# Performance work log

Hardware: AMD Instinct MI355X
Metric: run time of the kernel (lower is better)

Reference implementation:

```python
import jax, jax.numpy as jnp
import numpy as np

NUM_NODES = 100000
HIDDEN = 128
HEADS = 4
NUM_EDGES = 1600000
NUM_PAIRS = 100000


def _leaky_relu(x, slope=0.2):
    return jnp.where(x >= 0, x, slope * x)


def _gat_layer(x, W, a_src, a_dst, src, dst):
    # x: [N, D]; W: [D, H*Dh]; a_src/a_dst: [H, Dh]
    N = x.shape[0]
    H, Dh = a_src.shape
    h = (x @ W).reshape(N, H, Dh)
    hs = h[src]                                   # [E, H, Dh] gather
    e = _leaky_relu((hs * a_src).sum(-1) + (h[dst] * a_dst).sum(-1))  # [E, H]
    # torch scatter_reduce amax over a zeros buffer => max clamped at 0
    m = jnp.maximum(jax.ops.segment_max(e, dst, num_segments=N), 0.0)  # [N, H]
    a = jnp.exp(e - m[dst])
    s = jax.ops.segment_sum(a, dst, num_segments=N)
    a = a / (s[dst] + 1e-10)
    out = jax.ops.segment_sum(hs * a[..., None], dst, num_segments=N)  # [N, H, Dh]
    return out.reshape(N, H * Dh)


def setup_inputs() -> dict:
    key = jax.random.key(0)
    ks = jax.random.split(key, 16)
    N, D, H = NUM_NODES, HIDDEN, HEADS
    Dh = D // H
    sW = float(np.sqrt(6.0 / (D + D)))
    sa = float(np.sqrt(6.0 / (H + Dh)))
    inp = {
        'embed': jax.random.uniform(ks[0], (N, D), jnp.float32, -sW, sW),
        'W1': jax.random.uniform(ks[1], (D, D), jnp.float32, -sW, sW),
        'a_src1': jax.random.uniform(ks[2], (H, Dh), jnp.float32, -sa, sa),
        'a_dst1': jax.random.uniform(ks[3], (H, Dh), jnp.float32, -sa, sa),
        'W2': jax.random.uniform(ks[4], (D, D), jnp.float32, -sW, sW),
        'a_src2': jax.random.uniform(ks[5], (H, Dh), jnp.float32, -sa, sa),
        'a_dst2': jax.random.uniform(ks[6], (H, Dh), jnp.float32, -sa, sa),
        'lp_w1': jax.random.uniform(ks[7], (2 * D, D), jnp.float32, -sW, sW),
        'lp_b1': jnp.zeros((D,), jnp.float32),
        'lp_w2': jax.random.uniform(ks[8], (D, 1), jnp.float32, -sW, sW),
        'lp_b2': jnp.zeros((1,), jnp.float32),
        'edge_index': jax.random.randint(ks[9], (2, NUM_EDGES), 0, N, jnp.int64 if jax.config.jax_enable_x64 else jnp.int32),
        'link_src': jax.random.randint(ks[10], (NUM_PAIRS,), 0, N),
        'link_dst': jax.random.randint(ks[11], (NUM_PAIRS,), 0, N),
    }
    return inp


def reference(embed, W1, a_src1, a_dst1, W2, a_src2, a_dst2,
              lp_w1, lp_b1, lp_w2, lp_b2, edge_index, link_src, link_dst):
    src, dst = edge_index[0], edge_index[1]
    x = embed
    x = jax.nn.elu(_gat_layer(x, W1, a_src1, a_dst1, src, dst)) + x
    x = jax.nn.elu(_gat_layer(x, W2, a_src2, a_dst2, src, dst)) + x
    z = x
    hcat = jnp.concatenate([z[link_src], z[link_dst]], axis=-1)  # [P, 2D]
    hid = jax.nn.relu(hcat @ lp_w1 + lp_b1)
    logits = (hid @ lp_w2 + lp_b2).squeeze(-1)  # [P]
    return logits
```

## Files before the change

kernel.cpp:

```cpp
#include <hip/hip_runtime.h>

typedef unsigned short u16;
typedef unsigned int u32;
typedef __attribute__((ext_vector_type(8))) short short8;
typedef __attribute__((ext_vector_type(4))) float float4v;

#define N_NODES 100000
#define N_EDGES 1600000
#define N_PAIRS 100000
#define NBUCKP 256
#define NB_USED 196
#define BUCK_CAP 8704
#define BIN_GRID 391

__device__ __forceinline__ float bf2f(u32 lo16) {
    union { u32 u; float f; } v;
    v.u = lo16 << 16;
    return v.f;
}
__device__ __forceinline__ u16 f2bf(float f) {
    union { float f; u32 u; } v;
    v.f = f;
    u32 r = v.u + 0x7fffu + ((v.u >> 16) & 1u);
    return (u16)(r >> 16);
}

__global__ __launch_bounds__(256) void k_prepB4(const float* __restrict__ W1, const float* __restrict__ W2,
                                                const float* __restrict__ WA, const float* __restrict__ WB,
                                                u16* __restrict__ B1, u16* __restrict__ B2,
                                                u16* __restrict__ BA, u16* __restrict__ BB,
                                                int* __restrict__ bucket_cur) {
    if (blockIdx.x == 32) {
        bucket_cur[threadIdx.x] = threadIdx.x * BUCK_CAP;
        return;
    }
    int w = blockIdx.x >> 3;
    const float* W = (w == 0) ? W1 : (w == 1) ? W2 : (w == 2) ? WA : WB;
    u16* Bf = (w == 0) ? B1 : (w == 1) ? B2 : (w == 2) ? BA : BB;
    int t = (blockIdx.x & 7) * 256 + threadIdx.x;
    int kk = t >> 9, tn = (t >> 6) & 7, quad = (t >> 4) & 3, l15 = t & 15;
#pragma unroll
    for (int j = 0; j < 8; j++) {
        int k = kk * 32 + quad * 8 + j;
        int n = tn * 16 + l15;
        Bf[(size_t)t * 8 + j] = f2bf(W[k * 128 + n]);
    }
}

__global__ __launch_bounds__(256) void k_bin(const int* __restrict__ esrc, const int* __restrict__ edst,
                                             int* bucket_cur, int2* __restrict__ binned) {
    __shared__ int cnt[NBUCKP];
    __shared__ int base[NBUCKP];
    int t = threadIdx.x;
    cnt[t] = 0;
    __syncthreads();
    int s[16], d[16], r[16];
    int e0 = blockIdx.x * 4096;
#pragma unroll
    for (int k = 0; k < 16; k++) {
        int e = e0 + k * 256 + t;
        if (e < N_EDGES) {
            s[k] = esrc[e];
            d[k] = edst[e];
            r[k] = atomicAdd(&cnt[d[k] >> 9], 1);
        } else {
            d[k] = -1;
        }
    }
    __syncthreads();
    base[t] = cnt[t] ? atomicAdd(&bucket_cur[t], cnt[t]) : 0;
    __syncthreads();
#pragma unroll
    for (int k = 0; k < 16; k++) {
        if (d[k] >= 0) {
            int bk = d[k] >> 9;
            int pos = base[bk] + r[k];
            if (pos < (bk + 1) * BUCK_CAP)
                binned[pos] = make_int2(s[k], d[k]);
        }
    }
}

__global__ __launch_bounds__(512) void k_sort(const int2* __restrict__ binned,
                                              const int* __restrict__ bucket_cur,
                                              int* __restrict__ row_ptr,
                                              int* __restrict__ col_src) {
    __shared__ int cnt[512];
    __shared__ int sm[512];
    int b = blockIdx.x, t = threadIdx.x;

    int partial = 0;
    if (t < b) partial = bucket_cur[t] - t * BUCK_CAP;
    sm[t] = partial;
    __syncthreads();
    for (int o = 256; o >= 1; o >>= 1) {
        if (t < o) sm[t] += sm[t + o];
        __syncthreads();
    }
    int base = sm[0];
    int n_e = bucket_cur[b] - b * BUCK_CAP;
    if (n_e > BUCK_CAP) n_e = BUCK_CAP;
    __syncthreads();

    cnt[t] = 0;
    __syncthreads();
    const int2* ebase = binned + (size_t)b * BUCK_CAP;
    for (int i = t; i < n_e; i += 512)
        atomicAdd(&cnt[ebase[i].y & 511], 1);
    __syncthreads();
    int v = cnt[t];
    sm[t] = v;
    __syncthreads();
    for (int o = 1; o < 512; o <<= 1) {
        int x = (t >= o) ? sm[t - o] : 0;
        __syncthreads();
        sm[t] += x;
        __syncthreads();
    }
    int excl = base + sm[t] - v;
    int node = b * 512 + t;
    if (node <= N_NODES) row_ptr[node] = excl;
    cnt[t] = excl;
    __syncthreads();
    for (int i = t; i < n_e; i += 512) {
        int2 sd = ebase[i];
        int p = atomicAdd(&cnt[sd.y & 511], 1);
        col_src[p] = sd.x;
    }
}

template<bool AF32, bool DUAL, bool QUANT>
__global__ __launch_bounds__(256) void k_gemm(const void* __restrict__ Ap,
                                              const u16* __restrict__ Bf,
                                              const u16* __restrict__ Bf2,
                                              u16* __restrict__ C,
                                              u16* __restrict__ C2,
                                              char* __restrict__ hq,
                                              float* __restrict__ alsc,
                                              const float* __restrict__ a_src,
                                              const float* __restrict__ a_dst,
                                              float* __restrict__ al_d, int M) {
    int wave = threadIdx.x >> 6, lane = threadIdx.x & 63;
    int quad = lane >> 4, l15 = lane & 15;
    int row0 = blockIdx.x * 64 + wave * 16;
    int m = row0 + l15;
    int mload = (m < M) ? m : (M - 1);

    short8 a[4];
    if (AF32) {
        const float* A = (const float*)Ap;
#pragma unroll
        for (int kk = 0; kk < 4; kk++) {
            const float* p = A + (size_t)mload * 128 + kk * 32 + quad * 8;
            float4 f0 = *(const float4*)p;
            float4 f1 = *(const float4*)(p + 4);
            short8 av;
            av[0] = (short)f2bf(f0.x); av[1] = (short)f2bf(f0.y);
            av[2] = (short)f2bf(f0.z); av[3] = (short)f2bf(f0.w);
            av[4] = (short)f2bf(f1.x); av[5] = (short)f2bf(f1.y);
            av[6] = (short)f2bf(f1.z); av[7] = (short)f2bf(f1.w);
            a[kk] = av;
        }
    } else {
        const u16* A = (const u16*)Ap;
#pragma unroll
        for (int kk = 0; kk < 4; kk++)
            a[kk] = *(const short8*)(A + (size_t)mload * 128 + kk * 32 + quad * 8);
    }

    float4v acc[8], acc2[8];
#pragma unroll
    for (int tn = 0; tn < 8; tn++) {
        acc[tn] = (float4v){0.f, 0.f, 0.f, 0.f};
        if (DUAL) acc2[tn] = (float4v){0.f, 0.f, 0.f, 0.f};
    }

#pragma unroll
    for (int kk = 0; kk < 4; kk++) {
#pragma unroll
        for (int tn = 0; tn < 8; tn++) {
            short8 b = *(const short8*)(Bf + ((size_t)((kk * 8 + tn) * 64 + lane)) * 8);
            acc[tn] = __builtin_amdgcn_mfma_f32_16x16x32_bf16(a[kk], b, acc[tn], 0, 0, 0);
            if (DUAL) {
                short8 b2 = *(const short8*)(Bf2 + ((size_t)((kk * 8 + tn) * 64 + lane)) * 8);
                acc2[tn] = __builtin_amdgcn_mfma_f32_16x16x32_bf16(a[kk], b2, acc2[tn], 0, 0, 0);
            }
        }
    }

    float as0[4], as1[4], ad0[4], ad1[4];
    if (QUANT) {
#pragma unroll
        for (int hd = 0; hd < 4; hd++) {
            as0[hd] = a_src[hd * 32 + l15];
            as1[hd] = a_src[hd * 32 + 16 + l15];
            ad0[hd] = a_dst[hd * 32 + l15];
            ad1[hd] = a_dst[hd * 32 + 16 + l15];
        }
    }

#pragma unroll
    for (int rg = 0; rg < 4; rg++) {
        int gr = row0 + quad * 4 + rg;
        bool ok = (gr < M);
        if (!QUANT) {
            if (ok) {
#pragma unroll
                for (int tn = 0; tn < 8; tn++) {
                    C[(size_t)gr * 128 + tn * 16 + l15] = f2bf(acc[tn][rg]);
                    if (DUAL) C2[(size_t)gr * 128 + tn * 16 + l15] = f2bf(acc2[tn][rg]);
                }
            }
        } else {
            float amax = 0.f;
#pragma unroll
            for (int tn = 0; tn < 8; tn++) amax = fmaxf(amax, fabsf(acc[tn][rg]));
#pragma unroll
            for (int mm = 1; mm < 16; mm <<= 1) amax = fmaxf(amax, __shfl_xor(amax, mm, 64));
            float inv_s = (amax > 0.f) ? 127.f / amax : 0.f;
            if (ok) {
#pragma unroll
                for (int tn = 0; tn < 8; tn++) {
                    int q = (int)rintf(acc[tn][rg] * inv_s);
                    hq[(size_t)gr * 128 + tn * 16 + l15] = (char)q;
                }
                if (l15 == 0) alsc[(size_t)gr * 8 + 4] = amax * (1.f / 127.f);
            }
            float ps[4], pd[4];
#pragma unroll
            for (int hd = 0; hd < 4; hd++) {
                float c0 = acc[2 * hd][rg];
                float c1 = acc[2 * hd + 1][rg];
                ps[hd] = c0 * as0[hd] + c1 * as1[hd];
                pd[hd] = c0 * ad0[hd] + c1 * ad1[hd];
            }
#pragma unroll
            for (int mm = 1; mm < 16; mm <<= 1) {
#pragma unroll
                for (int hd = 0; hd < 4; hd++) {
                    ps[hd] += __shfl_xor(ps[hd], mm, 64);
                    pd[hd] += __shfl_xor(pd[hd], mm, 64);
                }
            }
            if (ok && l15 < 4) {
                float vs = (l15 == 0) ? ps[0] : (l15 == 1) ? ps[1] : (l15 == 2) ? ps[2] : ps[3];
                float vd = (l15 == 0) ? pd[0] : (l15 == 1) ? pd[1] : (l15 == 2) ? pd[2] : pd[3];
                alsc[(size_t)gr * 8 + l15] = vs;
                al_d[gr * 4 + l15] = vd;
            }
        }
    }
}

template<bool XF32>
__global__ __launch_bounds__(256) void k_agg(const int* __restrict__ row_ptr, const int* __restrict__ col_src,
                      const float* __restrict__ alsc, const float* __restrict__ al_d,
                      const char* __restrict__ hq,
                      const void* __restrict__ xin, u16* __restrict__ xout) {
    int node = blockIdx.x * 4 + (threadIdx.x >> 6);
    int lane = threadIdx.x & 63;
    int l15 = lane & 15;
    int grp = lane >> 4;
    int bh  = l15 >> 2;
    int ae  = lane >> 2;
    int ah  = lane & 3;
    int beg = row_ptr[node], end = row_ptr[node + 1];
    int deg = end - beg;
    int degm1 = (deg > 0) ? deg - 1 : 0;
    float adst = al_d[node * 4 + ah];
    const char* hrow = hq + l15 * 8;

    float sw = 0.f;
    float acc[8];
#pragma unroll
    for (int k = 0; k < 8; k++) acc[k] = 0.f;

    int nch = (deg + 15) >> 4;
    for (int cb = 0; cb < nch; cb++) {
        int c = cb * 16;
        int idx = c + l15;
        idx = (idx <= degm1) ? idx : degm1;
        int sv = col_src[beg + idx];

        int sA = __shfl(sv, ae, 64);
        const float* ap = alsc + (size_t)sA * 8;
        float ev = ap[ah] + adst;
        ev = fmaxf(ev, 0.2f * ev);
        float w = __expf(ev);
        w = ((c + ae) < deg) ? w : 0.f;
        sw += w;
        float wsc = w * ap[4];

#pragma unroll
        for (int i = 0; i < 4; i++) {
            int slot = 4 * i + grp;
            int s = __shfl(sv, slot, 64);
            float wl = __shfl(wsc, slot * 4 + bh, 64);
            uint2 hv = *(const uint2*)(hrow + (size_t)s * 128);
            acc[0] += wl * (float)(int)(signed char)(hv.x);
            acc[1] += wl * (float)(int)(signed char)(hv.x >> 8);
            acc[2] += wl * (float)(int)(signed char)(hv.x >> 16);
            acc[3] += wl * (float)(int)(signed char)(hv.x >> 24);
            acc[4] += wl * (float)(int)(signed char)(hv.y);
            acc[5] += wl * (float)(int)(signed char)(hv.y >> 8);
            acc[6] += wl * (float)(int)(signed char)(hv.y >> 16);
            acc[7] += wl * (float)(int)(signed char)(hv.y >> 24);
        }
    }

#pragma unroll
    for (int mm = 4; mm < 64; mm <<= 1) sw += __shfl_xor(sw, mm, 64);
    float inv = 1.f / (__shfl(sw, bh, 64) + 1e-10f);

#pragma unroll
    for (int k = 0; k < 8; k++) {
        acc[k] += __shfl_xor(acc[k], 16, 64);
        acc[k] += __shfl_xor(acc[k], 32, 64);
    }

    if (grp == 0) {
        float r[8];
        if (XF32) {
            const float* x = (const float*)xin;
            float4 x0 = *(const float4*)&x[(size_t)node * 128 + l15 * 8];
            float4 x1 = *(const float4*)&x[(size_t)node * 128 + l15 * 8 + 4];
            r[0] = x0.x; r[1] = x0.y; r[2] = x0.z; r[3] = x0.w;
            r[4] = x1.x; r[5] = x1.y; r[6] = x1.z; r[7] = x1.w;
        } else {
            const u16* x = (const u16*)xin;
            short8 xv = *(const short8*)&x[(size_t)node * 128 + l15 * 8];
#pragma unroll
            for (int k = 0; k < 8; k++) r[k] = bf2f((u16)xv[k]);
        }
        u32 ow[4];
#pragma unroll
        for (int k = 0; k < 4; k++) {
            float a0 = acc[2 * k] * inv;
            float a1 = acc[2 * k + 1] * inv;
            a0 = (a0 > 0.f) ? a0 : (__expf(a0) - 1.f);
            a1 = (a1 > 0.f) ? a1 : (__expf(a1) - 1.f);
            ow[k] = (u32)f2bf(a0 + r[2 * k]) | ((u32)f2bf(a1 + r[2 * k + 1]) << 16);
        }
        *(uint4*)&xout[(size_t)node * 128 + l15 * 8] = make_uint4(ow[0], ow[1], ow[2], ow[3]);
    }
}

__global__ void k_pair(const int* __restrict__ psrc, const int* __restrict__ pdst,
                       const u16* __restrict__ u, const u16* __restrict__ v,
                       const float* __restrict__ b1, const float* __restrict__ w2,
                       const float* __restrict__ b2, float* __restrict__ out) {
    int p = blockIdx.x * 4 + (threadIdx.x >> 6);
    int lane = threadIdx.x & 63;
    int s = psrc[p], d = pdst[p];
    float h0 = bf2f(u[(size_t)s * 128 + lane * 2])     + bf2f(v[(size_t)d * 128 + lane * 2])     + b1[lane * 2];
    float h1 = bf2f(u[(size_t)s * 128 + lane * 2 + 1]) + bf2f(v[(size_t)d * 128 + lane * 2 + 1]) + b1[lane * 2 + 1];
    h0 = (h0 > 0.f) ? h0 : 0.f;
    h1 = (h1 > 0.f) ? h1 : 0.f;
    float acc = h0 * w2[lane * 2] + h1 * w2[lane * 2 + 1];
#pragma unroll
    for (int m = 1; m < 64; m <<= 1) acc += __shfl_xor(acc, m, 64);
    if (lane == 0) out[p] = acc + b2[0];
}

extern "C" void kernel_launch(void* const* d_in, const int* in_sizes, int n_in,
                              void* d_out, int out_size, void* d_ws, size_t ws_size,
                              hipStream_t stream) {
    const float* embed  = (const float*)d_in[0];
    const float* W1     = (const float*)d_in[1];
    const float* a_src1 = (const float*)d_in[2];
    const float* a_dst1 = (const float*)d_in[3];
    const float* W2     = (const float*)d_in[4];
    const float* a_src2 = (const float*)d_in[5];
    const float* a_dst2 = (const float*)d_in[6];
    const float* lp_w1  = (const float*)d_in[7];
    const float* lp_b1  = (const float*)d_in[8];
    const float* lp_w2  = (const float*)d_in[9];
    const float* lp_b2  = (const float*)d_in[10];
    const int*   edge   = (const int*)d_in[11];
    const int*   lsrc   = (const int*)d_in[12];
    const int*   ldst   = (const int*)d_in[13];
    float* out = (float*)d_out;

    char* ws = (char*)d_ws;
    size_t off = 0;
    auto alloc = [&](size_t bytes) -> char* {
        char* p = ws + off;
        off += (bytes + 255) & ~(size_t)255;
        return p;
    };
    int*  row_ptr    = (int*)alloc((N_NODES + 1) * 4);
    int*  bucket_cur = (int*)alloc(NBUCKP * 4);
    int2* binned     = (int2*)alloc((size_t)NBUCKP * BUCK_CAP * 8);
    int*  col_src    = (int*)alloc((size_t)N_EDGES * 4);
    char* hq         = (char*)alloc((size_t)N_NODES * 128);
    float* alsc      = (float*)alloc((size_t)N_NODES * 8 * 4);
    float* al_d      = (float*)alloc((size_t)N_NODES * 4 * 4);
    u16*  x1         = (u16*)alloc((size_t)N_NODES * 128 * 2);
    u16*  z          = (u16*)alloc((size_t)N_NODES * 128 * 2);
    u16*  uu         = (u16*)alloc((size_t)N_NODES * 128 * 2);
    u16*  vv         = (u16*)alloc((size_t)N_NODES * 128 * 2);
    u16*  Bf1        = (u16*)alloc(128 * 128 * 2);
    u16*  Bf2        = (u16*)alloc(128 * 128 * 2);
    u16*  BfA        = (u16*)alloc(128 * 128 * 2);
    u16*  BfB        = (u16*)alloc(128 * 128 * 2);

    const int* esrc = edge;
    const int* edst = edge + N_EDGES;
    const int GB = (N_NODES + 63) / 64;

    k_prepB4<<<33, 256, 0, stream>>>(W1, W2, lp_w1, lp_w1 + 128 * 128, Bf1, Bf2, BfA, BfB, bucket_cur);

    k_bin <<<BIN_GRID, 256, 0, stream>>>(esrc, edst, bucket_cur, binned);
    k_sort<<<NB_USED, 512, 0, stream>>>(binned, bucket_cur, row_ptr, col_src);

    k_gemm<true, false, true><<<GB, 256, 0, stream>>>(embed, Bf1, nullptr, nullptr, nullptr,
                                                      hq, alsc, a_src1, a_dst1, al_d, N_NODES);
    k_agg<true><<<N_NODES / 4, 256, 0, stream>>>(row_ptr, col_src, alsc, al_d, hq, embed, x1);
    k_gemm<false, false, true><<<GB, 256, 0, stream>>>(x1, Bf2, nullptr, nullptr, nullptr,
                                                       hq, alsc, a_src2, a_dst2, al_d, N_NODES);
    k_agg<false><<<N_NODES / 4, 256, 0, stream>>>(row_ptr, col_src, alsc, al_d, hq, x1, z);
    k_gemm<false, true, false><<<GB, 256, 0, stream>>>(z, BfA, BfB, uu, vv,
                                                       nullptr, nullptr, nullptr, nullptr, nullptr, N_NODES);
    k_pair<<<N_PAIRS / 4, 256, 0, stream>>>(lsrc, ldst, uu, vv, lp_b1, lp_w2, lp_b2, out);
}
```

Before: 359.7 us.

## Use offset-int8 with fp16 magic-number unpack and v_fma_mix in aggregation

Stores quantized features with a +128 bias so that a byte permute with 0x64 produces fp16 values of 1024+128+q directly, avoiding per-byte sign-extension and int-to-float conversions. The weight is converted to fp16 once per load and accumulated with v_fma_mix_f32, and the constant offset (1152 times the weight sum) is subtracted at the end. The per-node scale is interleaved next to each head's attention logit so a single float2 load fetches both. Rounding the weight to fp16 and the large-offset cancellation reduce precision.

```diff
diff --git a/kernel.cpp b/kernel.cpp
--- a/kernel.cpp
+++ b/kernel.cpp
@@ -24,6 +24,9 @@
     u32 r = v.u + 0x7fffu + ((v.u >> 16) & 1u);
     return (u16)(r >> 16);
 }
+
+#define FMIX_LO(A, Q, W) asm("v_fma_mix_f32 %0, %1, %2, %0 op_sel:[0,0,0] op_sel_hi:[1,1,0]" : "+v"(A) : "v"(Q), "v"(W))
+#define FMIX_HI(A, Q, W) asm("v_fma_mix_f32 %0, %1, %2, %0 op_sel:[1,0,0] op_sel_hi:[1,1,0]" : "+v"(A) : "v"(Q), "v"(W))
 
 __global__ __launch_bounds__(256) void k_prepB4(const float* __restrict__ W1, const float* __restrict__ W2,
                                                 const float* __restrict__ WA, const float* __restrict__ WB,
@@ -222,9 +225,8 @@
 #pragma unroll
                 for (int tn = 0; tn < 8; tn++) {
                     int q = (int)rintf(acc[tn][rg] * inv_s);
-                    hq[(size_t)gr * 128 + tn * 16 + l15] = (char)q;
+                    hq[(size_t)gr * 128 + tn * 16 + l15] = (char)(q + 128);
                 }
-                if (l15 == 0) alsc[(size_t)gr * 8 + 4] = amax * (1.f / 127.f);
             }
             float ps[4], pd[4];
 #pragma unroll
@@ -245,7 +247,8 @@
             if (ok && l15 < 4) {
                 float vs = (l15 == 0) ? ps[0] : (l15 == 1) ? ps[1] : (l15 == 2) ? ps[2] : ps[3];
                 float vd = (l15 == 0) ? pd[0] : (l15 == 1) ? pd[1] : (l15 == 2) ? pd[2] : pd[3];
-                alsc[(size_t)gr * 8 + l15] = vs;
+                alsc[(size_t)gr * 8 + l15 * 2]     = vs;
+                alsc[(size_t)gr * 8 + l15 * 2 + 1] = amax * (1.f / 127.f);
                 al_d[gr * 4 + l15] = vd;
             }
         }
@@ -268,9 +271,10 @@
     int deg = end - beg;
     int degm1 = (deg > 0) ? deg - 1 : 0;
     float adst = al_d[node * 4 + ah];
-    const char* hrow = hq + l15 * 8;
-
-    float sw = 0.f;
+    u32 loff = (u32)(l15 * 8);
+
+    float sw = 0.f, swl = 0.f;
+    u32 h_one = 0x3C00u;
     float acc[8];
 #pragma unroll
     for (int k = 0; k < 8; k++) acc[k] = 0.f;
@@ -283,30 +287,37 @@
         int sv = col_src[beg + idx];
 
         int sA = __shfl(sv, ae, 64);
-        const float* ap = alsc + (size_t)sA * 8;
-        float ev = ap[ah] + adst;
+        float2 av = *(const float2*)(alsc + ((size_t)sA << 3) + (ah << 1));
+        float ev = av.x + adst;
         ev = fmaxf(ev, 0.2f * ev);
         float w = __expf(ev);
         w = ((c + ae) < deg) ? w : 0.f;
         sw += w;
-        float wsc = w * ap[4];
+        float wsc = w * av.y;
 
 #pragma unroll
         for (int i = 0; i < 4; i++) {
             int slot = 4 * i + grp;
             int s = __shfl(sv, slot, 64);
             float wl = __shfl(wsc, slot * 4 + bh, 64);
-            uint2 hv = *(const uint2*)(hrow + (size_t)s * 128);
-            acc[0] += wl * (float)(int)(signed char)(hv.x);
-            acc[1] += wl * (float)(int)(signed char)(hv.x >> 8);
-            acc[2] += wl * (float)(int)(signed char)(hv.x >> 16);
-            acc[3] += wl * (float)(int)(signed char)(hv.x >> 24);
-            acc[4] += wl * (float)(int)(signed char)(hv.y);
-            acc[5] += wl * (float)(int)(signed char)(hv.y >> 8);
-            acc[6] += wl * (float)(int)(signed char)(hv.y >> 16);
-            acc[7] += wl * (float)(int)(signed char)(hv.y >> 24);
-        }
-    }
+            u32 wlh;
+            asm("v_cvt_f16_f32 %0, %1" : "=v"(wlh) : "v"(wl));
+            FMIX_LO(swl, h_one, wlh);
+            u32 off = ((u32)s << 7) + loff;
+            uint2 hv = *(const uint2*)(hq + off);
+            u32 p01 = __builtin_amdgcn_perm(0x64646464u, hv.x, 0x04010400u);
+            u32 p23 = __builtin_amdgcn_perm(0x64646464u, hv.x, 0x04030402u);
+            u32 p45 = __builtin_amdgcn_perm(0x64646464u, hv.y, 0x04010400u);
+            u32 p67 = __builtin_amdgcn_perm(0x64646464u, hv.y, 0x04030402u);
+            FMIX_LO(acc[0], p01, wlh); FMIX_HI(acc[1], p01, wlh);
+            FMIX_LO(acc[2], p23, wlh); FMIX_HI(acc[3], p23, wlh);
+            FMIX_LO(acc[4], p45, wlh); FMIX_HI(acc[5], p45, wlh);
+            FMIX_LO(acc[6], p67, wlh); FMIX_HI(acc[7], p67, wlh);
+        }
+    }
+
+#pragma unroll
+    for (int k = 0; k < 8; k++) acc[k] = fmaf(swl, -1152.f, acc[k]);
 
 #pragma unroll
     for (int mm = 4; mm < 64; mm <<= 1) sw += __shfl_xor(sw, mm, 64);
```

Result: no change. 356.2 us (-1.0%).
